# Kernel tuning notes

Measured on AMD Instinct MI355X. Metric: run time of the kernel, lower is better.

The kernel has to match this reference:

```python
import jax, jax.numpy as jnp
import numpy as np

B, C, DM, H = 2, 256, 512, 8
D = DM // H          # d_head = 64
SPARSE_K = 64


def setup_inputs() -> dict:
    key = jax.random.key(0)
    ks = jax.random.split(key, 12)
    s = 0.02
    return {
        "x": jax.random.normal(ks[0], (B, C, DM), dtype=jnp.float32),
        "Wq": jax.random.normal(ks[1], (DM, DM), dtype=jnp.float32) * s,
        "bq": jnp.zeros((DM,), jnp.float32),
        "Wk": jax.random.normal(ks[2], (DM, DM), dtype=jnp.float32) * s,
        "bk": jnp.zeros((DM,), jnp.float32),
        "Wv": jax.random.normal(ks[3], (DM, DM), dtype=jnp.float32) * s,
        "bv": jnp.zeros((DM,), jnp.float32),
        "w1": jax.random.normal(ks[4], (D, 3 * D), dtype=jnp.float32) * s,
        "b1": jax.random.normal(ks[5], (D,), dtype=jnp.float32) * s,
        "w2": jax.random.normal(ks[6], (1, D), dtype=jnp.float32) * s,
        "b2": jax.random.normal(ks[7], (1,), dtype=jnp.float32) * s,
        "Wo": jax.random.normal(ks[8], (DM, DM), dtype=jnp.float32) * s,
        "bo": jnp.zeros((DM,), jnp.float32),
    }


def _heads(x, W, b):
    # torch Linear: x @ W.T + b, then (B,C,H,d) -> (B,H,C,d)
    y = jnp.einsum("bcD,ED->bcE", x, W) + b
    return y.reshape(B, C, H, D).transpose(0, 2, 1, 3)


def reference(x, Wq, bq, Wk, bk, Wv, bv, w1, b1, w2, b2, Wo, bo):
    q = _heads(x, Wq, bq)  # (B,H,C,d)
    k = _heads(x, Wk, bk)
    v = _heads(x, Wv, bv)

    # split first MLP layer weight: [:, :d] acts on q, [:, d:2d] on k, [:, 2d:] on q*k
    q_p = jnp.einsum("bhcd,ed->bhce", q, w1[:, :D])
    k_p = jnp.einsum("bhcd,ed->bhce", k, w1[:, D:2 * D])

    # res: (B,H,C,C,d)
    res = q_p[:, :, :, None, :] + k_p[:, :, None, :, :] + b1
    interaction = q[:, :, :, None, :] * k[:, :, None, :, :]
    res = res + jnp.einsum("bhije,fe->bhijf", interaction, w1[:, 2 * D:])

    # second MLP layer -> scalar score per pair, exact (erf) GELU as torch default
    h = jax.nn.gelu(res, approximate=False)
    scores = (jnp.einsum("bhijd,od->bhijo", h, w2) + b2)[..., 0]
    scores = scores / jnp.sqrt(jnp.float32(D))

    if SPARSE_K < C:
        top_vals = jax.lax.top_k(scores, SPARSE_K)[0]
        thresh = top_vals[..., -1:]
        scores = jnp.where(scores >= thresh, scores, jnp.float32(-1e9))

    attn = jax.nn.softmax(scores, axis=-1)  # dropout is identity (p=0 / eval)
    out = jnp.einsum("bhij,bhjd->bhid", attn, v)
    out = out.transpose(0, 2, 1, 3).reshape(B, C, DM)
    return jnp.einsum("bcD,ED->bcE", out, Wo) + bo
```

## Files before the change

### kernel.cpp

```cpp
#include <hip/hip_runtime.h>
#include <math.h>

typedef __bf16 bf16;
typedef __attribute__((ext_vector_type(4))) __bf16 bf16x4;
typedef __attribute__((ext_vector_type(8))) __bf16 bf16x8;
typedef __attribute__((ext_vector_type(4))) float floatx4;

__device__ __forceinline__ float gelu_exact(float x) {
    float tt = x * 0.70710678118654752440f;
    float e;
    if (__builtin_expect(fabsf(tt) > 0.5f, 0)) {
        e = erff(tt);
    } else {
        float s = tt * tt;
        e = tt * fmaf(s, fmaf(s, fmaf(s, fmaf(s, fmaf(s,
                -8.548327023450852e-4f, 5.223977625442188e-3f),
                -2.6866170645131252e-2f), 0.11283791670955126f),
                -0.3761263890318375f), 1.1283791670955126f);
    }
    return 0.5f * x * (1.0f + e);
}

__device__ __forceinline__ void split3(float a, bf16& h, bf16& m, bf16& l) {
    h = (bf16)a;  float r1 = a - (float)h;
    m = (bf16)r1; float r2 = r1 - (float)m;
    l = (bf16)r2;
}

struct SplitArgs {
    const float* src[5];
    bf16* h[5]; bf16* m[5]; bf16* l[5];
};

__global__ __launch_bounds__(256) void split3_512_kernel(SplitArgs S) {
    int z = blockIdx.z;
    const float* src = S.src[z];
    bf16* dh = S.h[z]; bf16* dm = S.m[z]; bf16* dl = S.l[z];
    int t = blockIdx.x * 256 + threadIdx.x;
    int row = t >> 7, kq = (t & 127) * 4;
    int rt = row >> 4, rm = row & 15;
    int ks = kq >> 5, q4 = (kq >> 3) & 3, u0 = kq & 7;
    int dst = ((rt * 16 + ks) * 64 + q4 * 16 + rm) * 8 + u0;
    float4 vv = *(const float4*)&src[row * 512 + kq];
    float a4[4] = {vv.x, vv.y, vv.z, vv.w};
    bf16x4 h, m, l;
    #pragma unroll
    for (int u = 0; u < 4; u++) {
        bf16 hh, mm, ll;
        split3(a4[u], hh, mm, ll);
        h[u] = hh; m[u] = mm; l[u] = ll;
    }
    *(bf16x4*)&dh[dst] = h;
    *(bf16x4*)&dm[dst] = m;
    *(bf16x4*)&dl[dst] = l;
}

struct MM2Args {
    const bf16 *Ah, *Am, *Al;
    const bf16 *Wh[3], *Wm[3], *Wl[3];
    const float* bias[3];
    float* outf[3];
    bf16 *kh, *km, *kl;
    int mode[3];
};

__global__ __launch_bounds__(64) void mm_mfma_kernel(MM2Args A) {
    const int z = blockIdx.z;
    const bf16* Wh = A.Wh[z]; const bf16* Wm = A.Wm[z]; const bf16* Wl = A.Wl[z];
    const float* bias = A.bias[z];
    const int lane = threadIdx.x;
    const int m16 = lane & 15, q4 = lane >> 4;
    const int mt = blockIdx.y, bx = blockIdx.x;

    floatx4 acc;
    {
        float bv = bias[bx * 16 + m16];
        acc[0] = bv; acc[1] = bv; acc[2] = bv; acc[3] = bv;
    }

    #pragma unroll 4
    for (int ks = 0; ks < 16; ks++) {
        int sa = ((mt * 16 + ks) * 64 + lane) * 8;
        bf16x8 ah = *(const bf16x8*)&A.Ah[sa];
        bf16x8 am = *(const bf16x8*)&A.Am[sa];
        bf16x8 al = *(const bf16x8*)&A.Al[sa];
        int sw = ((bx * 16 + ks) * 64 + lane) * 8;
        bf16x8 wh = *(const bf16x8*)&Wh[sw];
        bf16x8 wm = *(const bf16x8*)&Wm[sw];
        bf16x8 wl = *(const bf16x8*)&Wl[sw];
        acc = __builtin_amdgcn_mfma_f32_16x16x32_bf16(ah, wh, acc, 0, 0, 0);
        acc = __builtin_amdgcn_mfma_f32_16x16x32_bf16(ah, wm, acc, 0, 0, 0);
        acc = __builtin_amdgcn_mfma_f32_16x16x32_bf16(am, wh, acc, 0, 0, 0);
        acc = __builtin_amdgcn_mfma_f32_16x16x32_bf16(ah, wl, acc, 0, 0, 0);
        acc = __builtin_amdgcn_mfma_f32_16x16x32_bf16(al, wh, acc, 0, 0, 0);
        acc = __builtin_amdgcn_mfma_f32_16x16x32_bf16(am, wm, acc, 0, 0, 0);
    }

    const int mode = A.mode[z];
    const int n = bx * 16 + m16;
    #pragma unroll
    for (int r = 0; r < 4; r++) {
        int m = mt * 16 + q4 * 4 + r;
        float val = acc[r];
        if (mode == 0) {
            A.outf[z][m * 512 + n] = val;
        } else if (mode == 1) {
            A.outf[z][(((m >> 8) * 8 + (n >> 6)) * 256 + (m & 255)) * 64 + (n & 63)] = val;
        } else {
            int krow = ((m >> 8) * 8 + (n >> 6)) * 256 + (m & 255);
            int d = n & 63;
            int dst = (((krow >> 4) * 2 + (d >> 5)) * 64 + ((d >> 3) & 3) * 16 + (krow & 15)) * 8 + (d & 7);
            bf16 h, mm, l;
            split3(val, h, mm, l);
            A.kh[dst] = h; A.km[dst] = mm; A.kl[dst] = l;
        }
    }
}

__global__ __launch_bounds__(256, 3) void fused_mfma_attn_kernel(
    const float* __restrict__ q, const float* __restrict__ v,
    const bf16* __restrict__ khi, const bf16* __restrict__ kmid, const bf16* __restrict__ klo,
    const float* __restrict__ w1, const float* __restrict__ b1,
    const float* __restrict__ w2, const float* __restrict__ b2,
    bf16* __restrict__ oh, bf16* __restrict__ om, bf16* __restrict__ ol)
{
    const int i2 = blockIdx.x;
    const int bh = blockIdx.y;
    const int t  = threadIdx.x;
    const int lane = t & 63, w = t >> 6;
    const int m16 = lane & 15, q4 = lane >> 4;

    __shared__ float part[2][4][256];
    __shared__ float sc[2][256];
    __shared__ float qpb_s[2][64];
    __shared__ float sbuf[2][256];
    __shared__ float red[2][4][64];
    __shared__ float red2[2][4];
    __shared__ float thr_s[2], smax_s[2];

    const int f = w * 16 + m16;
    const float* w1row = w1 + f * 192;

    bf16x8 Ah[2][2], Am[2][2], Al[2][2];
    #pragma unroll
    for (int i01 = 0; i01 < 2; i01++) {
        const float* qrow = q + (bh * 256 + i2 * 2 + i01) * 64;
        float qa = 0.f;
        #pragma unroll
        for (int ks = 0; ks < 2; ks++) {
            int e0 = ks * 32 + q4 * 8;
            #pragma unroll
            for (int u = 0; u < 2; u++) {
                int e = e0 + u * 4;
                float4 wa = *(const float4*)&w1row[e];
                float4 wb = *(const float4*)&w1row[64 + e];
                float4 wc = *(const float4*)&w1row[128 + e];
                float4 qv = *(const float4*)&qrow[e];
                qa += wa.x * qv.x + wa.y * qv.y + wa.z * qv.z + wa.w * qv.w;
                float av[4];
                av[0] = fmaf(wc.x, qv.x, wb.x);
                av[1] = fmaf(wc.y, qv.y, wb.y);
                av[2] = fmaf(wc.z, qv.z, wb.z);
                av[3] = fmaf(wc.w, qv.w, wb.w);
                #pragma unroll
                for (int uu = 0; uu < 4; uu++) {
                    bf16 h, m, l;
                    split3(av[uu], h, m, l);
                    Ah[i01][ks][u * 4 + uu] = h;
                    Am[i01][ks][u * 4 + uu] = m;
                    Al[i01][ks][u * 4 + uu] = l;
                }
            }
        }
        qa += __shfl_xor(qa, 16);
        qa += __shfl_xor(qa, 32);
        if (lane < 16) qpb_s[i01][w * 16 + lane] = qa + b1[w * 16 + lane];
    }
    __syncthreads();

    floatx4 qpbr[2];
    qpbr[0] = *(const floatx4*)&qpb_s[0][w * 16 + q4 * 4];
    qpbr[1] = *(const floatx4*)&qpb_s[1][w * 16 + q4 * 4];
    const float4 w2f = *(const float4*)&w2[w * 16 + q4 * 4];
    const float b2v = b2[0];

    #pragma unroll 2
    for (int jt = 0; jt < 16; jt++) {
        int base = ((bh * 16 + jt) * 2 * 64 + lane) * 8;
        bf16x8 Kh0 = *(const bf16x8*)&khi [base];
        bf16x8 Km0 = *(const bf16x8*)&kmid[base];
        bf16x8 Kl0 = *(const bf16x8*)&klo [base];
        bf16x8 Kh1 = *(const bf16x8*)&khi [base + 512];
        bf16x8 Km1 = *(const bf16x8*)&kmid[base + 512];
        bf16x8 Kl1 = *(const bf16x8*)&klo [base + 512];
        #pragma unroll
        for (int i01 = 0; i01 < 2; i01++) {
            floatx4 a = qpbr[i01];
            a = __builtin_amdgcn_mfma_f32_16x16x32_bf16(Ah[i01][0], Kh0, a, 0, 0, 0);
            a = __builtin_amdgcn_mfma_f32_16x16x32_bf16(Ah[i01][0], Km0, a, 0, 0, 0);
            a = __builtin_amdgcn_mfma_f32_16x16x32_bf16(Am[i01][0], Kh0, a, 0, 0, 0);
            a = __builtin_amdgcn_mfma_f32_16x16x32_bf16(Ah[i01][0], Kl0, a, 0, 0, 0);
            a = __builtin_amdgcn_mfma_f32_16x16x32_bf16(Al[i01][0], Kh0, a, 0, 0, 0);
            a = __builtin_amdgcn_mfma_f32_16x16x32_bf16(Am[i01][0], Km0, a, 0, 0, 0);
            a = __builtin_amdgcn_mfma_f32_16x16x32_bf16(Ah[i01][1], Kh1, a, 0, 0, 0);
            a = __builtin_amdgcn_mfma_f32_16x16x32_bf16(Ah[i01][1], Km1, a, 0, 0, 0);
            a = __builtin_amdgcn_mfma_f32_16x16x32_bf16(Am[i01][1], Kh1, a, 0, 0, 0);
            a = __builtin_amdgcn_mfma_f32_16x16x32_bf16(Ah[i01][1], Kl1, a, 0, 0, 0);
            a = __builtin_amdgcn_mfma_f32_16x16x32_bf16(Al[i01][1], Kh1, a, 0, 0, 0);
            a = __builtin_amdgcn_mfma_f32_16x16x32_bf16(Am[i01][1], Km1, a, 0, 0, 0);
            float s = 0.f;
            s = fmaf(w2f.x, gelu_exact(a[0]), s);
            s = fmaf(w2f.y, gelu_exact(a[1]), s);
            s = fmaf(w2f.z, gelu_exact(a[2]), s);
            s = fmaf(w2f.w, gelu_exact(a[3]), s);
            s += __shfl_xor(s, 16);
            s += __shfl_xor(s, 32);
            if (lane < 16) part[i01][w][jt * 16 + lane] = s;
        }
    }
    __syncthreads();

    float score[2];
    #pragma unroll
    for (int i01 = 0; i01 < 2; i01++) {
        score[i01] = (((part[i01][0][t] + part[i01][1][t]) +
                       (part[i01][2][t] + part[i01][3][t])) + b2v) * 0.125f;
    }

    float sv0 = score[0], sv1 = score[1];
    #pragma unroll
    for (int k = 2; k <= 256; k <<= 1) {
        #pragma unroll
        for (int j = k >> 1; j >= 1; j >>= 1) {
            float pv0, pv1;
            if (j >= 64) {
                sbuf[0][t] = sv0; sbuf[1][t] = sv1;
                __syncthreads();
                pv0 = sbuf[0][t ^ j]; pv1 = sbuf[1][t ^ j];
                __syncthreads();
            } else {
                pv0 = __shfl_xor(sv0, j);
                pv1 = __shfl_xor(sv1, j);
            }
            bool keepMin = (((t & j) == 0) == ((t & k) == 0));
            sv0 = keepMin ? fminf(sv0, pv0) : fmaxf(sv0, pv0);
            sv1 = keepMin ? fminf(sv1, pv1) : fmaxf(sv1, pv1);
        }
    }
    if (t == 192) { thr_s[0] = sv0; thr_s[1] = sv1; }
    if (t == 255) { smax_s[0] = sv0; smax_s[1] = sv1; }
    __syncthreads();

    float p0 = (score[0] >= thr_s[0]) ? __expf(score[0] - smax_s[0]) : 0.0f;
    float p1 = (score[1] >= thr_s[1]) ? __expf(score[1] - smax_s[1]) : 0.0f;
    sc[0][t] = p0; sc[1][t] = p1;
    float ps0 = p0, ps1 = p1;
    #pragma unroll
    for (int mask = 1; mask < 64; mask <<= 1) {
        ps0 += __shfl_xor(ps0, mask);
        ps1 += __shfl_xor(ps1, mask);
    }
    if (lane == 0) { red2[0][w] = ps0; red2[1][w] = ps1; }
    __syncthreads();
    const float inv0 = 1.0f / ((red2[0][0] + red2[0][1]) + (red2[0][2] + red2[0][3]));
    const float inv1 = 1.0f / ((red2[1][0] + red2[1][1]) + (red2[1][2] + red2[1][3]));

    const int d = t & 63, g = t >> 6;
    const float* vb = v + bh * 256 * 64;
    float a0 = 0.f, a1 = 0.f;
    for (int j4 = 0; j4 < 16; j4++) {
        int jj = g * 64 + j4 * 4;
        float4 p40 = *(const float4*)&sc[0][jj];
        float4 p41 = *(const float4*)&sc[1][jj];
        float v0 = vb[(jj + 0) * 64 + d];
        float v1 = vb[(jj + 1) * 64 + d];
        float v2 = vb[(jj + 2) * 64 + d];
        float v3 = vb[(jj + 3) * 64 + d];
        a0 = fmaf(p40.x, v0, a0); a1 = fmaf(p41.x, v0, a1);
        a0 = fmaf(p40.y, v1, a0); a1 = fmaf(p41.y, v1, a1);
        a0 = fmaf(p40.z, v2, a0); a1 = fmaf(p41.z, v2, a1);
        a0 = fmaf(p40.w, v3, a0); a1 = fmaf(p41.w, v3, a1);
    }
    red[0][g][d] = a0; red[1][g][d] = a1;
    __syncthreads();

    if (t < 128) {
        int i01 = t >> 6, dd = t & 63;
        float o = ((red[i01][0][dd] + red[i01][1][dd]) +
                   (red[i01][2][dd] + red[i01][3][dd])) * (i01 ? inv1 : inv0);
        int b = bh >> 3, h = bh & 7;
        int row = b * 256 + i2 * 2 + i01;
        int n = h * 64 + dd;
        int dst = (((row >> 4) * 16 + (n >> 5)) * 64 + ((n >> 3) & 3) * 16 + (row & 15)) * 8 + (n & 7);
        bf16 hh, mm, ll;
        split3(o, hh, mm, ll);
        oh[dst] = hh; om[dst] = mm; ol[dst] = ll;
    }
}

extern "C" void kernel_launch(void* const* d_in, const int* in_sizes, int n_in,
                              void* d_out, int out_size, void* d_ws, size_t ws_size,
                              hipStream_t stream) {
    const float* x  = (const float*)d_in[0];
    const float* Wq = (const float*)d_in[1];
    const float* bq = (const float*)d_in[2];
    const float* Wk = (const float*)d_in[3];
    const float* bk = (const float*)d_in[4];
    const float* Wv = (const float*)d_in[5];
    const float* bv = (const float*)d_in[6];
    const float* w1 = (const float*)d_in[7];
    const float* b1 = (const float*)d_in[8];
    const float* w2 = (const float*)d_in[9];
    const float* b2 = (const float*)d_in[10];
    const float* Wo = (const float*)d_in[11];
    const float* bo = (const float*)d_in[12];
    float* out = (float*)d_out;

    const int NE = 262144;
    float* qb  = (float*)d_ws;
    float* vb  = qb + NE;
    bf16* base = (bf16*)(vb + NE);
    bf16* khi  = base;            bf16* kmid = khi + NE;    bf16* klo = kmid + NE;
    bf16* xs   = klo + NE;
    bf16* wqs  = xs  + 3 * NE;
    bf16* wks  = wqs + 3 * NE;
    bf16* wvs  = wks + 3 * NE;
    bf16* wos  = wvs + 3 * NE;
    bf16* oas  = wos + 3 * NE;

    {
        SplitArgs S;
        const float* srcs[5] = {x, Wq, Wk, Wv, Wo};
        bf16* dsts[5] = {xs, wqs, wks, wvs, wos};
        for (int z = 0; z < 5; z++) {
            S.src[z] = srcs[z];
            S.h[z] = dsts[z]; S.m[z] = dsts[z] + NE; S.l[z] = dsts[z] + 2 * NE;
        }
        split3_512_kernel<<<dim3(256, 1, 5), 256, 0, stream>>>(S);
    }
    {
        MM2Args M;
        M.Ah = xs; M.Am = xs + NE; M.Al = xs + 2 * NE;
        M.Wh[0] = wqs; M.Wm[0] = wqs + NE; M.Wl[0] = wqs + 2 * NE;
        M.Wh[1] = wks; M.Wm[1] = wks + NE; M.Wl[1] = wks + 2 * NE;
        M.Wh[2] = wvs; M.Wm[2] = wvs + NE; M.Wl[2] = wvs + 2 * NE;
        M.bias[0] = bq; M.bias[1] = bk; M.bias[2] = bv;
        M.outf[0] = qb; M.outf[1] = nullptr; M.outf[2] = vb;
        M.kh = khi; M.km = kmid; M.kl = klo;
        M.mode[0] = 1; M.mode[1] = 2; M.mode[2] = 1;
        mm_mfma_kernel<<<dim3(32, 32, 3), 64, 0, stream>>>(M);
    }
    fused_mfma_attn_kernel<<<dim3(128, 16), 256, 0, stream>>>(
        qb, vb, khi, kmid, klo, w1, b1, w2, b2,
        oas, oas + NE, oas + 2 * NE);
    {
        MM2Args M;
        M.Ah = oas; M.Am = oas + NE; M.Al = oas + 2 * NE;
        M.Wh[0] = wos; M.Wm[0] = wos + NE; M.Wl[0] = wos + 2 * NE;
        M.Wh[1] = wos; M.Wm[1] = wos; M.Wl[1] = wos;
        M.Wh[2] = wos; M.Wm[2] = wos; M.Wl[2] = wos;
        M.bias[0] = bo; M.bias[1] = bo; M.bias[2] = bo;
        M.outf[0] = out; M.outf[1] = out; M.outf[2] = out;
        M.kh = khi; M.km = kmid; M.kl = klo;
        M.mode[0] = 0; M.mode[1] = 0; M.mode[2] = 0;
        mm_mfma_kernel<<<dim3(32, 32, 1), 64, 0, stream>>>(M);
    }
}
```

Before: 183.2 us.

## Pack paired-row math into float2 ops and split MFMA accumulator chains

Rewrites the GELU, score reduction, bitonic sort, softmax and PV accumulation to operate on two-wide float vectors, so the compiler can emit packed FP32 instructions covering both query rows at once. The MFMA dependency chains in the projection GEMM and the score kernel are split across two independent accumulators to shorten the serial dependency latency. The GELU now always evaluates the polynomial and patches in erff only for large inputs, which adds some redundant work. Shared-memory arrays are interleaved as float2, which changes the bank access patterns.

```diff
diff --git a/kernel.cpp b/kernel.cpp
--- a/kernel.cpp
+++ b/kernel.cpp
@@ -5,20 +5,24 @@
 typedef __attribute__((ext_vector_type(4))) __bf16 bf16x4;
 typedef __attribute__((ext_vector_type(8))) __bf16 bf16x8;
 typedef __attribute__((ext_vector_type(4))) float floatx4;
-
-__device__ __forceinline__ float gelu_exact(float x) {
-    float tt = x * 0.70710678118654752440f;
-    float e;
-    if (__builtin_expect(fabsf(tt) > 0.5f, 0)) {
-        e = erff(tt);
-    } else {
-        float s = tt * tt;
-        e = tt * fmaf(s, fmaf(s, fmaf(s, fmaf(s, fmaf(s,
-                -8.548327023450852e-4f, 5.223977625442188e-3f),
-                -2.6866170645131252e-2f), 0.11283791670955126f),
-                -0.3761263890318375f), 1.1283791670955126f);
-    }
-    return 0.5f * x * (1.0f + e);
+typedef __attribute__((ext_vector_type(2))) float f32x2;
+
+__device__ __forceinline__ f32x2 mk2(float a, float b) { f32x2 r; r.x = a; r.y = b; return r; }
+__device__ __forceinline__ f32x2 sp2(float a) { f32x2 r; r.x = a; r.y = a; return r; }
+
+__device__ __forceinline__ f32x2 gelu2(f32x2 x) {
+    f32x2 tt = x * 0.70710678118654752440f;
+    f32x2 s  = tt * tt;
+    f32x2 p  = __builtin_elementwise_fma(s, sp2(-8.548327023450852e-4f), sp2(5.223977625442188e-3f));
+    p = __builtin_elementwise_fma(s, p, sp2(-2.6866170645131252e-2f));
+    p = __builtin_elementwise_fma(s, p, sp2(0.11283791670955126f));
+    p = __builtin_elementwise_fma(s, p, sp2(-0.3761263890318375f));
+    p = __builtin_elementwise_fma(s, p, sp2(1.1283791670955126f));
+    f32x2 e = tt * p;
+    if (__builtin_expect(fabsf(tt.x) > 0.5f, 0)) e.x = erff(tt.x);
+    if (__builtin_expect(fabsf(tt.y) > 0.5f, 0)) e.y = erff(tt.y);
+    f32x2 hx = x * 0.5f;
+    return __builtin_elementwise_fma(hx, e, hx);
 }
 
 __device__ __forceinline__ void split3(float a, bf16& h, bf16& m, bf16& l) {
@@ -72,10 +76,11 @@
     const int m16 = lane & 15, q4 = lane >> 4;
     const int mt = blockIdx.y, bx = blockIdx.x;
 
-    floatx4 acc;
+    floatx4 acc0, acc1;
     {
         float bv = bias[bx * 16 + m16];
-        acc[0] = bv; acc[1] = bv; acc[2] = bv; acc[3] = bv;
+        acc0[0] = bv; acc0[1] = bv; acc0[2] = bv; acc0[3] = bv;
+        acc1[0] = 0.f; acc1[1] = 0.f; acc1[2] = 0.f; acc1[3] = 0.f;
     }
 
     #pragma unroll 4
@@ -88,13 +93,14 @@
         bf16x8 wh = *(const bf16x8*)&Wh[sw];
         bf16x8 wm = *(const bf16x8*)&Wm[sw];
         bf16x8 wl = *(const bf16x8*)&Wl[sw];
-        acc = __builtin_amdgcn_mfma_f32_16x16x32_bf16(ah, wh, acc, 0, 0, 0);
-        acc = __builtin_amdgcn_mfma_f32_16x16x32_bf16(ah, wm, acc, 0, 0, 0);
-        acc = __builtin_amdgcn_mfma_f32_16x16x32_bf16(am, wh, acc, 0, 0, 0);
-        acc = __builtin_amdgcn_mfma_f32_16x16x32_bf16(ah, wl, acc, 0, 0, 0);
-        acc = __builtin_amdgcn_mfma_f32_16x16x32_bf16(al, wh, acc, 0, 0, 0);
-        acc = __builtin_amdgcn_mfma_f32_16x16x32_bf16(am, wm, acc, 0, 0, 0);
-    }
+        acc0 = __builtin_amdgcn_mfma_f32_16x16x32_bf16(ah, wh, acc0, 0, 0, 0);
+        acc1 = __builtin_amdgcn_mfma_f32_16x16x32_bf16(ah, wm, acc1, 0, 0, 0);
+        acc0 = __builtin_amdgcn_mfma_f32_16x16x32_bf16(am, wh, acc0, 0, 0, 0);
+        acc1 = __builtin_amdgcn_mfma_f32_16x16x32_bf16(ah, wl, acc1, 0, 0, 0);
+        acc0 = __builtin_amdgcn_mfma_f32_16x16x32_bf16(al, wh, acc0, 0, 0, 0);
+        acc1 = __builtin_amdgcn_mfma_f32_16x16x32_bf16(am, wm, acc1, 0, 0, 0);
+    }
+    floatx4 acc = acc0 + acc1;
 
     const int mode = A.mode[z];
     const int n = bx * 16 + m16;
@@ -130,13 +136,13 @@
     const int lane = t & 63, w = t >> 6;
     const int m16 = lane & 15, q4 = lane >> 4;
 
-    __shared__ float part[2][4][256];
-    __shared__ float sc[2][256];
+    __shared__ f32x2 part2[4][256];
+    __shared__ f32x2 sc2[256];
     __shared__ float qpb_s[2][64];
-    __shared__ float sbuf[2][256];
-    __shared__ float red[2][4][64];
-    __shared__ float red2[2][4];
-    __shared__ float thr_s[2], smax_s[2];
+    __shared__ f32x2 sbuf2[256];
+    __shared__ f32x2 red_s[4][64];
+    __shared__ f32x2 red2_s[4];
+    __shared__ f32x2 thr_s2, smax_s2;
 
     const int f = w * 16 + m16;
     const float* w1row = w1 + f * 192;
@@ -145,23 +151,20 @@
     #pragma unroll
     for (int i01 = 0; i01 < 2; i01++) {
         const float* qrow = q + (bh * 256 + i2 * 2 + i01) * 64;
-        float qa = 0.f;
+        floatx4 qacc;
+        qacc[0] = 0.f; qacc[1] = 0.f; qacc[2] = 0.f; qacc[3] = 0.f;
         #pragma unroll
         for (int ks = 0; ks < 2; ks++) {
             int e0 = ks * 32 + q4 * 8;
             #pragma unroll
             for (int u = 0; u < 2; u++) {
                 int e = e0 + u * 4;
-                float4 wa = *(const float4*)&w1row[e];
-                float4 wb = *(const float4*)&w1row[64 + e];
-                float4 wc = *(const float4*)&w1row[128 + e];
-                float4 qv = *(const float4*)&qrow[e];
-                qa += wa.x * qv.x + wa.y * qv.y + wa.z * qv.z + wa.w * qv.w;
-                float av[4];
-                av[0] = fmaf(wc.x, qv.x, wb.x);
-                av[1] = fmaf(wc.y, qv.y, wb.y);
-                av[2] = fmaf(wc.z, qv.z, wb.z);
-                av[3] = fmaf(wc.w, qv.w, wb.w);
+                floatx4 wa = *(const floatx4*)&w1row[e];
+                floatx4 wb = *(const floatx4*)&w1row[64 + e];
+                floatx4 wc = *(const floatx4*)&w1row[128 + e];
+                floatx4 qv = *(const floatx4*)&qrow[e];
+                qacc = __builtin_elementwise_fma(wa, qv, qacc);
+                floatx4 av = __builtin_elementwise_fma(wc, qv, wb);
                 #pragma unroll
                 for (int uu = 0; uu < 4; uu++) {
                     bf16 h, m, l;
@@ -172,6 +175,7 @@
                 }
             }
         }
+        float qa = (qacc[0] + qacc[1]) + (qacc[2] + qacc[3]);
         qa += __shfl_xor(qa, 16);
         qa += __shfl_xor(qa, 32);
         if (lane < 16) qpb_s[i01][w * 16 + lane] = qa + b1[w * 16 + lane];
@@ -181,7 +185,9 @@
     floatx4 qpbr[2];
     qpbr[0] = *(const floatx4*)&qpb_s[0][w * 16 + q4 * 4];
     qpbr[1] = *(const floatx4*)&qpb_s[1][w * 16 + q4 * 4];
-    const float4 w2f = *(const float4*)&w2[w * 16 + q4 * 4];
+    const floatx4 w2f = *(const floatx4*)&w2[w * 16 + q4 * 4];
+    const f32x2 w2a = mk2(w2f[0], w2f[1]);
+    const f32x2 w2b = mk2(w2f[2], w2f[3]);
     const float b2v = b2[0];
 
     #pragma unroll 2
@@ -193,101 +199,106 @@
         bf16x8 Kh1 = *(const bf16x8*)&khi [base + 512];
         bf16x8 Km1 = *(const bf16x8*)&kmid[base + 512];
         bf16x8 Kl1 = *(const bf16x8*)&klo [base + 512];
+        f32x2 sp;
         #pragma unroll
         for (int i01 = 0; i01 < 2; i01++) {
             floatx4 a = qpbr[i01];
-            a = __builtin_amdgcn_mfma_f32_16x16x32_bf16(Ah[i01][0], Kh0, a, 0, 0, 0);
-            a = __builtin_amdgcn_mfma_f32_16x16x32_bf16(Ah[i01][0], Km0, a, 0, 0, 0);
-            a = __builtin_amdgcn_mfma_f32_16x16x32_bf16(Am[i01][0], Kh0, a, 0, 0, 0);
-            a = __builtin_amdgcn_mfma_f32_16x16x32_bf16(Ah[i01][0], Kl0, a, 0, 0, 0);
-            a = __builtin_amdgcn_mfma_f32_16x16x32_bf16(Al[i01][0], Kh0, a, 0, 0, 0);
-            a = __builtin_amdgcn_mfma_f32_16x16x32_bf16(Am[i01][0], Km0, a, 0, 0, 0);
-            a = __builtin_amdgcn_mfma_f32_16x16x32_bf16(Ah[i01][1], Kh1, a, 0, 0, 0);
-            a = __builtin_amdgcn_mfma_f32_16x16x32_bf16(Ah[i01][1], Km1, a, 0, 0, 0);
-            a = __builtin_amdgcn_mfma_f32_16x16x32_bf16(Am[i01][1], Kh1, a, 0, 0, 0);
-            a = __builtin_amdgcn_mfma_f32_16x16x32_bf16(Ah[i01][1], Kl1, a, 0, 0, 0);
-            a = __builtin_amdgcn_mfma_f32_16x16x32_bf16(Al[i01][1], Kh1, a, 0, 0, 0);
-            a = __builtin_amdgcn_mfma_f32_16x16x32_bf16(Am[i01][1], Km1, a, 0, 0, 0);
-            float s = 0.f;
-            s = fmaf(w2f.x, gelu_exact(a[0]), s);
-            s = fmaf(w2f.y, gelu_exact(a[1]), s);
-            s = fmaf(w2f.z, gelu_exact(a[2]), s);
-            s = fmaf(w2f.w, gelu_exact(a[3]), s);
+            floatx4 a2;
+            a2[0] = 0.f; a2[1] = 0.f; a2[2] = 0.f; a2[3] = 0.f;
+            a  = __builtin_amdgcn_mfma_f32_16x16x32_bf16(Ah[i01][0], Kh0, a,  0, 0, 0);
+            a2 = __builtin_amdgcn_mfma_f32_16x16x32_bf16(Ah[i01][0], Km0, a2, 0, 0, 0);
+            a  = __builtin_amdgcn_mfma_f32_16x16x32_bf16(Am[i01][0], Kh0, a,  0, 0, 0);
+            a2 = __builtin_amdgcn_mfma_f32_16x16x32_bf16(Ah[i01][0], Kl0, a2, 0, 0, 0);
+            a  = __builtin_amdgcn_mfma_f32_16x16x32_bf16(Al[i01][0], Kh0, a,  0, 0, 0);
+            a2 = __builtin_amdgcn_mfma_f32_16x16x32_bf16(Am[i01][0], Km0, a2, 0, 0, 0);
+            a  = __builtin_amdgcn_mfma_f32_16x16x32_bf16(Ah[i01][1], Kh1, a,  0, 0, 0);
+            a2 = __builtin_amdgcn_mfma_f32_16x16x32_bf16(Ah[i01][1], Km1, a2, 0, 0, 0);
+            a  = __builtin_amdgcn_mfma_f32_16x16x32_bf16(Am[i01][1], Kh1, a,  0, 0, 0);
+            a2 = __builtin_amdgcn_mfma_f32_16x16x32_bf16(Ah[i01][1], Kl1, a2, 0, 0, 0);
+            a  = __builtin_amdgcn_mfma_f32_16x16x32_bf16(Al[i01][1], Kh1, a,  0, 0, 0);
+            a2 = __builtin_amdgcn_mfma_f32_16x16x32_bf16(Am[i01][1], Km1, a2, 0, 0, 0);
+            a = a + a2;
+            f32x2 g01 = gelu2(mk2(a[0], a[1]));
+            f32x2 g23 = gelu2(mk2(a[2], a[3]));
+            f32x2 sv2 = g01 * w2a;
+            sv2 = __builtin_elementwise_fma(g23, w2b, sv2);
+            float s = sv2.x + sv2.y;
             s += __shfl_xor(s, 16);
             s += __shfl_xor(s, 32);
-            if (lane < 16) part[i01][w][jt * 16 + lane] = s;
-        }
-    }
-    __syncthreads();
-
-    float score[2];
-    #pragma unroll
-    for (int i01 = 0; i01 < 2; i01++) {
-        score[i01] = (((part[i01][0][t] + part[i01][1][t]) +
-                       (part[i01][2][t] + part[i01][3][t])) + b2v) * 0.125f;
-    }
-
-    float sv0 = score[0], sv1 = score[1];
+            sp[i01] = s;
+        }
+        if (lane < 16) part2[w][jt * 16 + lane] = sp;
+    }
+    __syncthreads();
+
+    f32x2 score = ((part2[0][t] + part2[1][t]) + (part2[2][t] + part2[3][t]) + b2v) * 0.125f;
+
+    f32x2 sv = score;
     #pragma unroll
     for (int k = 2; k <= 256; k <<= 1) {
         #pragma unroll
         for (int j = k >> 1; j >= 1; j >>= 1) {
-            float pv0, pv1;
+            f32x2 pv;
             if (j >= 64) {
-                sbuf[0][t] = sv0; sbuf[1][t] = sv1;
+                sbuf2[t] = sv;
                 __syncthreads();
-                pv0 = sbuf[0][t ^ j]; pv1 = sbuf[1][t ^ j];
+                pv = sbuf2[t ^ j];
                 __syncthreads();
             } else {
-                pv0 = __shfl_xor(sv0, j);
-                pv1 = __shfl_xor(sv1, j);
+                pv.x = __shfl_xor(sv.x, j);
+                pv.y = __shfl_xor(sv.y, j);
             }
             bool keepMin = (((t & j) == 0) == ((t & k) == 0));
-            sv0 = keepMin ? fminf(sv0, pv0) : fmaxf(sv0, pv0);
-            sv1 = keepMin ? fminf(sv1, pv1) : fmaxf(sv1, pv1);
-        }
-    }
-    if (t == 192) { thr_s[0] = sv0; thr_s[1] = sv1; }
-    if (t == 255) { smax_s[0] = sv0; smax_s[1] = sv1; }
-    __syncthreads();
-
-    float p0 = (score[0] >= thr_s[0]) ? __expf(score[0] - smax_s[0]) : 0.0f;
-    float p1 = (score[1] >= thr_s[1]) ? __expf(score[1] - smax_s[1]) : 0.0f;
-    sc[0][t] = p0; sc[1][t] = p1;
-    float ps0 = p0, ps1 = p1;
+            f32x2 mn = __builtin_elementwise_min(sv, pv);
+            f32x2 mx = __builtin_elementwise_max(sv, pv);
+            sv = keepMin ? mn : mx;
+        }
+    }
+    if (t == 192) thr_s2  = sv;
+    if (t == 255) smax_s2 = sv;
+    __syncthreads();
+
+    float p0 = (score.x >= thr_s2.x) ? __expf(score.x - smax_s2.x) : 0.0f;
+    float p1 = (score.y >= thr_s2.y) ? __expf(score.y - smax_s2.y) : 0.0f;
+    sc2[t] = mk2(p0, p1);
+    f32x2 ps = mk2(p0, p1);
     #pragma unroll
     for (int mask = 1; mask < 64; mask <<= 1) {
-        ps0 += __shfl_xor(ps0, mask);
-        ps1 += __shfl_xor(ps1, mask);
-    }
-    if (lane == 0) { red2[0][w] = ps0; red2[1][w] = ps1; }
-    __syncthreads();
-    const float inv0 = 1.0f / ((red2[0][0] + red2[0][1]) + (red2[0][2] + red2[0][3]));
-    const float inv1 = 1.0f / ((red2[1][0] + red2[1][1]) + (red2[1][2] + red2[1][3]));
+        ps.x += __shfl_xor(ps.x, mask);
+        ps.y += __shfl_xor(ps.y, mask);
+    }
+    if (lane == 0) red2_s[w] = ps;
+    __syncthreads();
+    f32x2 den = (red2_s[0] + red2_s[1]) + (red2_s[2] + red2_s[3]);
+    f32x2 invp;
+    invp.x = 1.0f / den.x;
+    invp.y = 1.0f / den.y;
 
     const int d = t & 63, g = t >> 6;
     const float* vb = v + bh * 256 * 64;
-    float a0 = 0.f, a1 = 0.f;
+    f32x2 av = mk2(0.f, 0.f);
     for (int j4 = 0; j4 < 16; j4++) {
         int jj = g * 64 + j4 * 4;
-        float4 p40 = *(const float4*)&sc[0][jj];
-        float4 p41 = *(const float4*)&sc[1][jj];
+        f32x2 pp0 = sc2[jj + 0];
+        f32x2 pp1 = sc2[jj + 1];
+        f32x2 pp2 = sc2[jj + 2];
+        f32x2 pp3 = sc2[jj + 3];
         float v0 = vb[(jj + 0) * 64 + d];
         float v1 = vb[(jj + 1) * 64 + d];
         float v2 = vb[(jj + 2) * 64 + d];
         float v3 = vb[(jj + 3) * 64 + d];
-        a0 = fmaf(p40.x, v0, a0); a1 = fmaf(p41.x, v0, a1);
-        a0 = fmaf(p40.y, v1, a0); a1 = fmaf(p41.y, v1, a1);
-        a0 = fmaf(p40.z, v2, a0); a1 = fmaf(p41.z, v2, a1);
-        a0 = fmaf(p40.w, v3, a0); a1 = fmaf(p41.w, v3, a1);
-    }
-    red[0][g][d] = a0; red[1][g][d] = a1;
+        av = __builtin_elementwise_fma(pp0, sp2(v0), av);
+        av = __builtin_elementwise_fma(pp1, sp2(v1), av);
+        av = __builtin_elementwise_fma(pp2, sp2(v2), av);
+        av = __builtin_elementwise_fma(pp3, sp2(v3), av);
+    }
+    red_s[g][d] = av;
     __syncthreads();
 
     if (t < 128) {
         int i01 = t >> 6, dd = t & 63;
-        float o = ((red[i01][0][dd] + red[i01][1][dd]) +
-                   (red[i01][2][dd] + red[i01][3][dd])) * (i01 ? inv1 : inv0);
+        f32x2 osum = (red_s[0][dd] + red_s[1][dd]) + (red_s[2][dd] + red_s[3][dd]);
+        float o = (i01 ? osum.y : osum.x) * (i01 ? invp.y : invp.x);
         int b = bh >> 3, h = bh & 7;
         int row = b * 256 + i2 * 2 + i01;
         int n = h * 64 + dd;
```

Result: no change. 185.9 us (+1.5%).

## Replace bf16 triple split with fp16 double split for MFMA emulation

Applied to the files above, without the earlier changes.

Switches the fp32-emulation scheme from a three-way bf16 split (six MFMAs per product) to a two-way fp16 split (four MFMAs per product). The matmul and attention-score kernels now accumulate into two independent accumulators to shorten dependency chains, and the attention kernel's launch bound occupancy hint rises from 3 to 4 blocks. This cuts MFMA count, split-buffer memory traffic and register pressure. The cost is fp16's narrower exponent range, which risks precision loss or overflow for small or large values.

```diff
diff --git a/kernel.cpp b/kernel.cpp
--- a/kernel.cpp
+++ b/kernel.cpp
@@ -1,9 +1,9 @@
 #include <hip/hip_runtime.h>
 #include <math.h>
 
-typedef __bf16 bf16;
-typedef __attribute__((ext_vector_type(4))) __bf16 bf16x4;
-typedef __attribute__((ext_vector_type(8))) __bf16 bf16x8;
+typedef _Float16 fp16;
+typedef __attribute__((ext_vector_type(4))) _Float16 f16x4;
+typedef __attribute__((ext_vector_type(8))) _Float16 f16x8;
 typedef __attribute__((ext_vector_type(4))) float floatx4;
 
 __device__ __forceinline__ float gelu_exact(float x) {
@@ -21,21 +21,20 @@
     return 0.5f * x * (1.0f + e);
 }
 
-__device__ __forceinline__ void split3(float a, bf16& h, bf16& m, bf16& l) {
-    h = (bf16)a;  float r1 = a - (float)h;
-    m = (bf16)r1; float r2 = r1 - (float)m;
-    l = (bf16)r2;
+__device__ __forceinline__ void split2(float a, fp16& h, fp16& m) {
+    h = (fp16)a;
+    m = (fp16)(a - (float)h);
 }
 
 struct SplitArgs {
     const float* src[5];
-    bf16* h[5]; bf16* m[5]; bf16* l[5];
+    fp16* h[5]; fp16* m[5];
 };
 
-__global__ __launch_bounds__(256) void split3_512_kernel(SplitArgs S) {
+__global__ __launch_bounds__(256) void split2_512_kernel(SplitArgs S) {
     int z = blockIdx.z;
     const float* src = S.src[z];
-    bf16* dh = S.h[z]; bf16* dm = S.m[z]; bf16* dl = S.l[z];
+    fp16* dh = S.h[z]; fp16* dm = S.m[z];
     int t = blockIdx.x * 256 + threadIdx.x;
     int row = t >> 7, kq = (t & 127) * 4;
     int rt = row >> 4, rm = row & 15;
@@ -43,58 +42,55 @@
     int dst = ((rt * 16 + ks) * 64 + q4 * 16 + rm) * 8 + u0;
     float4 vv = *(const float4*)&src[row * 512 + kq];
     float a4[4] = {vv.x, vv.y, vv.z, vv.w};
-    bf16x4 h, m, l;
+    f16x4 h, m;
     #pragma unroll
     for (int u = 0; u < 4; u++) {
-        bf16 hh, mm, ll;
-        split3(a4[u], hh, mm, ll);
-        h[u] = hh; m[u] = mm; l[u] = ll;
-    }
-    *(bf16x4*)&dh[dst] = h;
-    *(bf16x4*)&dm[dst] = m;
-    *(bf16x4*)&dl[dst] = l;
+        fp16 hh, mm;
+        split2(a4[u], hh, mm);
+        h[u] = hh; m[u] = mm;
+    }
+    *(f16x4*)&dh[dst] = h;
+    *(f16x4*)&dm[dst] = m;
 }
 
 struct MM2Args {
-    const bf16 *Ah, *Am, *Al;
-    const bf16 *Wh[3], *Wm[3], *Wl[3];
+    const fp16 *Ah, *Am;
+    const fp16 *Wh[3], *Wm[3];
     const float* bias[3];
     float* outf[3];
-    bf16 *kh, *km, *kl;
+    fp16 *kh, *km;
     int mode[3];
 };
 
 __global__ __launch_bounds__(64) void mm_mfma_kernel(MM2Args A) {
     const int z = blockIdx.z;
-    const bf16* Wh = A.Wh[z]; const bf16* Wm = A.Wm[z]; const bf16* Wl = A.Wl[z];
+    const fp16* Wh = A.Wh[z]; const fp16* Wm = A.Wm[z];
     const float* bias = A.bias[z];
     const int lane = threadIdx.x;
     const int m16 = lane & 15, q4 = lane >> 4;
     const int mt = blockIdx.y, bx = blockIdx.x;
 
-    floatx4 acc;
+    floatx4 acc0, acc1;
     {
         float bv = bias[bx * 16 + m16];
-        acc[0] = bv; acc[1] = bv; acc[2] = bv; acc[3] = bv;
+        acc0[0] = bv; acc0[1] = bv; acc0[2] = bv; acc0[3] = bv;
+        acc1[0] = 0.f; acc1[1] = 0.f; acc1[2] = 0.f; acc1[3] = 0.f;
     }
 
     #pragma unroll 4
     for (int ks = 0; ks < 16; ks++) {
         int sa = ((mt * 16 + ks) * 64 + lane) * 8;
-        bf16x8 ah = *(const bf16x8*)&A.Ah[sa];
-        bf16x8 am = *(const bf16x8*)&A.Am[sa];
-        bf16x8 al = *(const bf16x8*)&A.Al[sa];
+        f16x8 ah = *(const f16x8*)&A.Ah[sa];
+        f16x8 am = *(const f16x8*)&A.Am[sa];
         int sw = ((bx * 16 + ks) * 64 + lane) * 8;
-        bf16x8 wh = *(const bf16x8*)&Wh[sw];
-        bf16x8 wm = *(const bf16x8*)&Wm[sw];
-        bf16x8 wl = *(const bf16x8*)&Wl[sw];
-        acc = __builtin_amdgcn_mfma_f32_16x16x32_bf16(ah, wh, acc, 0, 0, 0);
-        acc = __builtin_amdgcn_mfma_f32_16x16x32_bf16(ah, wm, acc, 0, 0, 0);
-        acc = __builtin_amdgcn_mfma_f32_16x16x32_bf16(am, wh, acc, 0, 0, 0);
-        acc = __builtin_amdgcn_mfma_f32_16x16x32_bf16(ah, wl, acc, 0, 0, 0);
-        acc = __builtin_amdgcn_mfma_f32_16x16x32_bf16(al, wh, acc, 0, 0, 0);
-        acc = __builtin_amdgcn_mfma_f32_16x16x32_bf16(am, wm, acc, 0, 0, 0);
-    }
+        f16x8 wh = *(const f16x8*)&Wh[sw];
+        f16x8 wm = *(const f16x8*)&Wm[sw];
+        acc0 = __builtin_amdgcn_mfma_f32_16x16x32_f16(ah, wh, acc0, 0, 0, 0);
+        acc1 = __builtin_amdgcn_mfma_f32_16x16x32_f16(ah, wm, acc1, 0, 0, 0);
+        acc0 = __builtin_amdgcn_mfma_f32_16x16x32_f16(am, wh, acc0, 0, 0, 0);
+        acc1 = __builtin_amdgcn_mfma_f32_16x16x32_f16(am, wm, acc1, 0, 0, 0);
+    }
+    floatx4 acc = acc0 + acc1;
 
     const int mode = A.mode[z];
     const int n = bx * 16 + m16;
@@ -110,19 +106,19 @@
             int krow = ((m >> 8) * 8 + (n >> 6)) * 256 + (m & 255);
             int d = n & 63;
             int dst = (((krow >> 4) * 2 + (d >> 5)) * 64 + ((d >> 3) & 3) * 16 + (krow & 15)) * 8 + (d & 7);
-            bf16 h, mm, l;
-            split3(val, h, mm, l);
-            A.kh[dst] = h; A.km[dst] = mm; A.kl[dst] = l;
-        }
-    }
-}
-
-__global__ __launch_bounds__(256, 3) void fused_mfma_attn_kernel(
+            fp16 h, mm;
+            split2(val, h, mm);
+            A.kh[dst] = h; A.km[dst] = mm;
+        }
+    }
+}
+
+__global__ __launch_bounds__(256, 4) void fused_mfma_attn_kernel(
     const float* __restrict__ q, const float* __restrict__ v,
-    const bf16* __restrict__ khi, const bf16* __restrict__ kmid, const bf16* __restrict__ klo,
+    const fp16* __restrict__ khi, const fp16* __restrict__ kmid,
     const float* __restrict__ w1, const float* __restrict__ b1,
     const float* __restrict__ w2, const float* __restrict__ b2,
-    bf16* __restrict__ oh, bf16* __restrict__ om, bf16* __restrict__ ol)
+    fp16* __restrict__ oh, fp16* __restrict__ om)
 {
     const int i2 = blockIdx.x;
     const int bh = blockIdx.y;
@@ -141,7 +137,7 @@
     const int f = w * 16 + m16;
     const float* w1row = w1 + f * 192;
 
-    bf16x8 Ah[2][2], Am[2][2], Al[2][2];
+    f16x8 Ah[2][2], Am[2][2];
     #pragma unroll
     for (int i01 = 0; i01 < 2; i01++) {
         const float* qrow = q + (bh * 256 + i2 * 2 + i01) * 64;
@@ -164,11 +160,10 @@
                 av[3] = fmaf(wc.w, qv.w, wb.w);
                 #pragma unroll
                 for (int uu = 0; uu < 4; uu++) {
-                    bf16 h, m, l;
-                    split3(av[uu], h, m, l);
+                    fp16 h, m;
+                    split2(av[uu], h, m);
                     Ah[i01][ks][u * 4 + uu] = h;
                     Am[i01][ks][u * 4 + uu] = m;
-                    Al[i01][ks][u * 4 + uu] = l;
                 }
             }
         }
@@ -187,27 +182,24 @@
     #pragma unroll 2
     for (int jt = 0; jt < 16; jt++) {
         int base = ((bh * 16 + jt) * 2 * 64 + lane) * 8;
-        bf16x8 Kh0 = *(const bf16x8*)&khi [base];
-        bf16x8 Km0 = *(const bf16x8*)&kmid[base];
-        bf16x8 Kl0 = *(const bf16x8*)&klo [base];
-        bf16x8 Kh1 = *(const bf16x8*)&khi [base + 512];
-        bf16x8 Km1 = *(const bf16x8*)&kmid[base + 512];
-        bf16x8 Kl1 = *(const bf16x8*)&klo [base + 512];
+        f16x8 Kh0 = *(const f16x8*)&khi [base];
+        f16x8 Km0 = *(const f16x8*)&kmid[base];
+        f16x8 Kh1 = *(const f16x8*)&khi [base + 512];
+        f16x8 Km1 = *(const f16x8*)&kmid[base + 512];
         #pragma unroll
         for (int i01 = 0; i01 < 2; i01++) {
             floatx4 a = qpbr[i01];
-            a = __builtin_amdgcn_mfma_f32_16x16x32_bf16(Ah[i01][0], Kh0, a, 0, 0, 0);
-            a = __builtin_amdgcn_mfma_f32_16x16x32_bf16(Ah[i01][0], Km0, a, 0, 0, 0);
-            a = __builtin_amdgcn_mfma_f32_16x16x32_bf16(Am[i01][0], Kh0, a, 0, 0, 0);
-            a = __builtin_amdgcn_mfma_f32_16x16x32_bf16(Ah[i01][0], Kl0, a, 0, 0, 0);
-            a = __builtin_amdgcn_mfma_f32_16x16x32_bf16(Al[i01][0], Kh0, a, 0, 0, 0);
-            a = __builtin_amdgcn_mfma_f32_16x16x32_bf16(Am[i01][0], Km0, a, 0, 0, 0);
-            a = __builtin_amdgcn_mfma_f32_16x16x32_bf16(Ah[i01][1], Kh1, a, 0, 0, 0);
-            a = __builtin_amdgcn_mfma_f32_16x16x32_bf16(Ah[i01][1], Km1, a, 0, 0, 0);
-            a = __builtin_amdgcn_mfma_f32_16x16x32_bf16(Am[i01][1], Kh1, a, 0, 0, 0);
-            a = __builtin_amdgcn_mfma_f32_16x16x32_bf16(Ah[i01][1], Kl1, a, 0, 0, 0);
-            a = __builtin_amdgcn_mfma_f32_16x16x32_bf16(Al[i01][1], Kh1, a, 0, 0, 0);
-            a = __builtin_amdgcn_mfma_f32_16x16x32_bf16(Am[i01][1], Km1, a, 0, 0, 0);
+            floatx4 a2;
+            a2[0] = 0.f; a2[1] = 0.f; a2[2] = 0.f; a2[3] = 0.f;
+            a  = __builtin_amdgcn_mfma_f32_16x16x32_f16(Ah[i01][0], Kh0, a,  0, 0, 0);
+            a2 = __builtin_amdgcn_mfma_f32_16x16x32_f16(Ah[i01][0], Km0, a2, 0, 0, 0);
+            a  = __builtin_amdgcn_mfma_f32_16x16x32_f16(Am[i01][0], Kh0, a,  0, 0, 0);
+            a2 = __builtin_amdgcn_mfma_f32_16x16x32_f16(Am[i01][0], Km0, a2, 0, 0, 0);
+            a  = __builtin_amdgcn_mfma_f32_16x16x32_f16(Ah[i01][1], Kh1, a,  0, 0, 0);
+            a2 = __builtin_amdgcn_mfma_f32_16x16x32_f16(Ah[i01][1], Km1, a2, 0, 0, 0);
+            a  = __builtin_amdgcn_mfma_f32_16x16x32_f16(Am[i01][1], Kh1, a,  0, 0, 0);
+            a2 = __builtin_amdgcn_mfma_f32_16x16x32_f16(Am[i01][1], Km1, a2, 0, 0, 0);
+            a = a + a2;
             float s = 0.f;
             s = fmaf(w2f.x, gelu_exact(a[0]), s);
             s = fmaf(w2f.y, gelu_exact(a[1]), s);
@@ -292,9 +284,9 @@
         int row = b * 256 + i2 * 2 + i01;
         int n = h * 64 + dd;
         int dst = (((row >> 4) * 16 + (n >> 5)) * 64 + ((n >> 3) & 3) * 16 + (row & 15)) * 8 + (n & 7);
-        bf16 hh, mm, ll;
-        split3(o, hh, mm, ll);
-        oh[dst] = hh; om[dst] = mm; ol[dst] = ll;
+        fp16 hh, mm;
+        split2(o, hh, mm);
+        oh[dst] = hh; om[dst] = mm;
     }
 }
 
@@ -319,49 +311,49 @@
     const int NE = 262144;
     float* qb  = (float*)d_ws;
     float* vb  = qb + NE;
-    bf16* base = (bf16*)(vb + NE);
-    bf16* khi  = base;            bf16* kmid = khi + NE;    bf16* klo = kmid + NE;
-    bf16* xs   = klo + NE;
-    bf16* wqs  = xs  + 3 * NE;
-    bf16* wks  = wqs + 3 * NE;
-    bf16* wvs  = wks + 3 * NE;
-    bf16* wos  = wvs + 3 * NE;
-    bf16* oas  = wos + 3 * NE;
+    fp16* base = (fp16*)(vb + NE);
+    fp16* khi  = base;            fp16* kmid = khi + NE;
+    fp16* xs   = kmid + NE;
+    fp16* wqs  = xs  + 2 * NE;
+    fp16* wks  = wqs + 2 * NE;
+    fp16* wvs  = wks + 2 * NE;
+    fp16* wos  = wvs + 2 * NE;
+    fp16* oas  = wos + 2 * NE;
 
     {
         SplitArgs S;
         const float* srcs[5] = {x, Wq, Wk, Wv, Wo};
-        bf16* dsts[5] = {xs, wqs, wks, wvs, wos};
+        fp16* dsts[5] = {xs, wqs, wks, wvs, wos};
         for (int z = 0; z < 5; z++) {
             S.src[z] = srcs[z];
-            S.h[z] = dsts[z]; S.m[z] = dsts[z] + NE; S.l[z] = dsts[z] + 2 * NE;
-        }
-        split3_512_kernel<<<dim3(256, 1, 5), 256, 0, stream>>>(S);
+            S.h[z] = dsts[z]; S.m[z] = dsts[z] + NE;
+        }
+        split2_512_kernel<<<dim3(256, 1, 5), 256, 0, stream>>>(S);
     }
     {
         MM2Args M;
-        M.Ah = xs; M.Am = xs + NE; M.Al = xs + 2 * NE;
-        M.Wh[0] = wqs; M.Wm[0] = wqs + NE; M.Wl[0] = wqs + 2 * NE;
-        M.Wh[1] = wks; M.Wm[1] = wks + NE; M.Wl[1] = wks + 2 * NE;
-        M.Wh[2] = wvs; M.Wm[2] = wvs + NE; M.Wl[2] = wvs + 2 * NE;
+        M.Ah = xs; M.Am = xs + NE;
+        M.Wh[0] = wqs; M.Wm[0] = wqs + NE;
+        M.Wh[1] = wks; M.Wm[1] = wks + NE;
+        M.Wh[2] = wvs; M.Wm[2] = wvs + NE;
         M.bias[0] = bq; M.bias[1] = bk; M.bias[2] = bv;
         M.outf[0] = qb; M.outf[1] = nullptr; M.outf[2] = vb;
-        M.kh = khi; M.km = kmid; M.kl = klo;
+        M.kh = khi; M.km = kmid;
         M.mode[0] = 1; M.mode[1] = 2; M.mode[2] = 1;
         mm_mfma_kernel<<<dim3(32, 32, 3), 64, 0, stream>>>(M);
     }
     fused_mfma_attn_kernel<<<dim3(128, 16), 256, 0, stream>>>(
-        qb, vb, khi, kmid, klo, w1, b1, w2, b2,
-        oas, oas + NE, oas + 2 * NE);
+        qb, vb, khi, kmid, w1, b1, w2, b2,
+        oas, oas + NE);
     {
         MM2Args M;
-        M.Ah = oas; M.Am = oas + NE; M.Al = oas + 2 * NE;
-        M.Wh[0] = wos; M.Wm[0] = wos + NE; M.Wl[0] = wos + 2 * NE;
-        M.Wh[1] = wos; M.Wm[1] = wos; M.Wl[1] = wos;
-        M.Wh[2] = wos; M.Wm[2] = wos; M.Wl[2] = wos;
+        M.Ah = oas; M.Am = oas + NE;
+        M.Wh[0] = wos; M.Wm[0] = wos + NE;
+        M.Wh[1] = wos; M.Wm[1] = wos;
+        M.Wh[2] = wos; M.Wm[2] = wos;
         M.bias[0] = bo; M.bias[1] = bo; M.bias[2] = bo;
         M.outf[0] = out; M.outf[1] = out; M.outf[2] = out;
-        M.kh = khi; M.km = kmid; M.kl = klo;
+        M.kh = khi; M.km = kmid;
         M.mode[0] = 0; M.mode[1] = 0; M.mode[2] = 0;
         mm_mfma_kernel<<<dim3(32, 32, 1), 64, 0, stream>>>(M);
     }
```

Result: faster. 177.2 us (-3.3%).
